# Optimization experiments

Hardware: AMD Instinct MI355X
Metric: run time of the kernel (lower is better)

The kernel has to match this reference:

```python
import jax, jax.numpy as jnp
import numpy as np

jax.config.update("jax_enable_x64", True)  # faithful int64 fixed-point requantize

B, K, N = 2048, 4096, 8192
INT32_MAX_MINUS = 2147418112  # threshold from multiply_by_quantize_mul


def setup_inputs() -> dict:
    key = jax.random.key(0)
    k1, k2, k3 = jax.random.split(key, 3)
    x = jax.random.randint(k1, (B, K), -128, 128, dtype=jnp.int8)
    weights = jax.random.randint(k2, (N, K), -128, 128, dtype=jnp.int8)
    bias = jax.random.randint(k3, (N, 1), -1024, 1024, dtype=jnp.int32)
    return {
        "x": x,
        "weights": weights,
        "bias": bias,
        "q_mantissa": 1431655765,   # ~2/3 in Q31 fixed point
        "exponent": -3,
        "output_zero_point": -5,
    }


def multiply_by_quantize_mul(x, q_mantissa, exponent):
    # Python precedence in original: (q_mantissa + (1<<15)) >> 16
    reduced_mantissa = ((q_mantissa + (1 << 15)) >> 16) if q_mantissa < INT32_MAX_MINUS else 32767
    total_shifts = 15 - exponent
    x = x * np.int64(reduced_mantissa)
    x = x + np.int64(1 << (total_shifts - 1))  # rounding term
    return jnp.right_shift(x, total_shifts)    # arithmetic shift on signed int64


def reference(x, weights, bias, q_mantissa, exponent, output_zero_point):
    # int8 GEMM accumulated in int32: result[b, n] = sum_k x[b, k] * w[n, k]
    acc = jnp.einsum("bk,nk->bn", x.astype(jnp.int32), weights.astype(jnp.int32))
    acc = acc + bias.T  # bias [N,1] -> [1,N], broadcast over batch
    acc = multiply_by_quantize_mul(acc.astype(jnp.int64), q_mantissa, exponent)
    acc = acc + np.int64(output_zero_point)
    out = jnp.clip(acc, -128, 127).astype(jnp.int8)
    return out
```

## Files before the change

### kernel.cpp

```cpp
#include <hip/hip_runtime.h>

#define DEVI __device__ __forceinline__

typedef int i32x4 __attribute__((ext_vector_type(4)));

static constexpr int Bdim = 2048;
static constexpr int Kdim = 4096;
static constexpr int Ndim = 8192;
static constexpr int BK   = 128;
static constexpr int NT   = Kdim / BK;

typedef __attribute__((address_space(1))) const unsigned int gas_t;
typedef __attribute__((address_space(3))) unsigned int las_t;

DEVI void gload_lds16(const void* g, void* l) {
    __builtin_amdgcn_global_load_lds((gas_t*)g, (las_t*)l, 16, 0, 0);
}

DEVI int pack4(i32x4 v) {
    return (v[0] & 255) | ((v[1] & 255) << 8) | ((v[2] & 255) << 16) | (v[3] << 24);
}

__global__ void pack_i32_to_i8(const int* __restrict__ in, char* __restrict__ out, int n16) {
    int i = blockIdx.x * blockDim.x + threadIdx.x;
    if (i >= n16) return;
    const i32x4* src = (const i32x4*)in + (size_t)i * 4;
    i32x4 r;
    r[0] = pack4(src[0]);
    r[1] = pack4(src[1]);
    r[2] = pack4(src[2]);
    r[3] = pack4(src[3]);
    ((i32x4*)out)[i] = r;
}

#define CFENCE asm volatile("" ::: "memory")
DEVI void bar() { CFENCE; __builtin_amdgcn_s_barrier(); CFENCE; }
#define WAITVM(N) asm volatile("s_waitcnt vmcnt(" #N ")" ::: "memory")
#define PRIO1 __builtin_amdgcn_s_setprio(1)
#define PRIO0 __builtin_amdgcn_s_setprio(0)

#define QUAD(MB)                                                                 \
    do {                                                                         \
        _Pragma("unroll") for (int mm = 0; mm < 4; ++mm)                         \
        _Pragma("unroll") for (int n = 0; n < 4; ++n)                            \
            acc[(MB) + mm][n] = __builtin_amdgcn_mfma_i32_16x16x64_i8(           \
                a[mm], b[n], acc[(MB) + mm][n], 0, 0, 0);                        \
    } while (0)

#define TILE(CUR, S1, S2, S3, S4, VM)                                                 \
    {                                                                                 \
        { _Pragma("unroll") for (int mm = 0; mm < 4; ++mm) a[mm] = rdA(CUR, 0, mm);   \
          _Pragma("unroll") for (int n = 0; n < 4; ++n)    b[n]  = rdB(CUR, 0, n);    \
          S1; bar(); PRIO1; QUAD(0); PRIO0; bar(); }                                  \
        { _Pragma("unroll") for (int mm = 0; mm < 4; ++mm) a[mm] = rdA(CUR, 0, 4+mm); \
          S2; bar(); PRIO1; QUAD(4); PRIO0; bar(); }                                  \
        { _Pragma("unroll") for (int mm = 0; mm < 4; ++mm) a[mm] = rdA(CUR, 1, mm);   \
          _Pragma("unroll") for (int n = 0; n < 4; ++n)    b[n]  = rdB(CUR, 1, n);    \
          S3; bar(); PRIO1; QUAD(0); PRIO0; bar(); }                                  \
        { _Pragma("unroll") for (int mm = 0; mm < 4; ++mm) a[mm] = rdA(CUR, 1, 4+mm); \
          S4; bar(); PRIO1; QUAD(4); PRIO0; VM; bar(); }                              \
    }

__global__ __launch_bounds__(512, 2)
void gemm8(const char* __restrict__ A8, const char* __restrict__ B8,
           const int* __restrict__ bias,
           const int* __restrict__ qm_p, const int* __restrict__ ex_p,
           const int* __restrict__ zp_p, int* __restrict__ out) {
    __shared__ i32x4 smem4[8192];
    char* smem = (char*)smem4;

    const int tid  = threadIdx.x;
    const int wid  = tid >> 6;
    const int lane = tid & 63;
    const int l15  = lane & 15;
    const int lks  = lane >> 4;
    const int wr   = wid >> 2;
    const int wc   = wid & 3;

    const int bid = blockIdx.x;
    const int swz = (bid & 7) * 32 + (bid >> 3);
    const int bm  = swz >> 5;
    const int bn  = swz & 31;
    const int arow0 = bm * 256;
    const int brow0 = bn * 256;

    const int swsel = lks ^ ((l15 >> 1) & 3);
    const int a_rd16 = (wr * 128 + l15) * 4 + swsel;
    const int b_rd16 = 4096 + (wc * 64 + l15) * 4 + swsel;

    const int st_c = (tid & 3) ^ ((tid >> 3) & 3);
    const char* agp = A8 + (size_t)(arow0 + (tid >> 2)) * Kdim + st_c * 16;
    const char* bgp = B8 + (size_t)(brow0 + (tid >> 2)) * Kdim + st_c * 16;

    auto stage = [&](int isb, int t, int ks) {
        const char* gp = (isb ? bgp : agp) + (size_t)t * BK + ks * 64;
        const int lb = (isb ? 65536 : 0) + (t & 1) * 32768 + ks * 16384 + tid * 16;
        gload_lds16(gp, &smem[lb]);
        gload_lds16(gp + (size_t)128 * Kdim, &smem[lb + 8192]);
    };
    auto rdA = [&](int buf, int ks, int m) {
        return smem4[buf * 2048 + ks * 1024 + a_rd16 + m * 64];
    };
    auto rdB = [&](int buf, int ks, int n) {
        return smem4[buf * 2048 + ks * 1024 + b_rd16 + n * 64];
    };

    i32x4 acc[8][4] = {};
    i32x4 a[4], b[4];

    stage(1, 0, 0); stage(0, 0, 0); stage(1, 0, 1); stage(0, 0, 1);
    stage(1, 1, 0); stage(0, 1, 0); stage(1, 1, 1);
    WAITVM(6);
    bar();

    int cur = 0;
    for (int t = 0; t < NT - 2; ++t) {
        TILE(cur,
             stage(0, t + 1, 1),
             stage(1, t + 2, 0),
             stage(0, t + 2, 0),
             stage(1, t + 2, 1),
             WAITVM(6));
        cur ^= 1;
    }
    TILE(cur,
         stage(0, NT - 1, 1),
         ((void)0), ((void)0), ((void)0),
         WAITVM(0));
    cur ^= 1;
    TILE(cur, ((void)0), ((void)0), ((void)0), ((void)0), ((void)0));

    const int qm = *qm_p;
    const int ex = *ex_p;
    const int zp = *zp_p;
    const int rm = (qm < 2147418112) ? ((qm + (1 << 15)) >> 16) : 32767;
    const int shifts = 15 - ex;
    const long long rnd = (shifts > 0) ? (1LL << (shifts - 1)) : 0;

    int bv[4];
#pragma unroll
    for (int n = 0; n < 4; ++n) bv[n] = bias[brow0 + wc * 64 + n * 16 + l15];

#pragma unroll
    for (int m = 0; m < 8; ++m) {
        const int row0 = arow0 + wr * 128 + m * 16 + lks * 4;
#pragma unroll
        for (int n = 0; n < 4; ++n) {
            const int col = brow0 + wc * 64 + n * 16 + l15;
#pragma unroll
            for (int j = 0; j < 4; ++j) {
                long long t = (long long)(acc[m][n][j] + bv[n]) * rm + rnd;
                t >>= shifts;
                t += zp;
                t = t < -128 ? -128 : (t > 127 ? 127 : t);
                out[(size_t)(row0 + j) * Ndim + col] = (int)t;
            }
        }
    }
}

extern "C" void kernel_launch(void* const* d_in, const int* in_sizes, int n_in,
                              void* d_out, int out_size, void* d_ws, size_t ws_size,
                              hipStream_t stream) {
    const int* x32  = (const int*)d_in[0];
    const int* w32  = (const int*)d_in[1];
    const int* bias = (const int*)d_in[2];
    const int* qm   = (const int*)d_in[3];
    const int* ex   = (const int*)d_in[4];
    const int* zp   = (const int*)d_in[5];
    int* out = (int*)d_out;

    char* xa = (char*)d_ws;
    char* wa = xa + (size_t)Bdim * Kdim;
    const int nx16 = Bdim * Kdim / 16;
    const int nw16 = Ndim * Kdim / 16;
    pack_i32_to_i8<<<(nx16 + 255) / 256, 256, 0, stream>>>(x32, xa, nx16);
    pack_i32_to_i8<<<(nw16 + 255) / 256, 256, 0, stream>>>(w32, wa, nw16);

    const int grid = (Bdim / 256) * (Ndim / 256);
    gemm8<<<grid, 512, 0, stream>>>(xa, wa, bias, qm, ex, zp, out);
}
```

Before: 105.5 us.

## Use 4-wave blocks with 128x128 per-wave tiles and simple double buffering

Replaces the 8-wave, 256x256 block kernel with a 4-wave version in which each wave computes a 128x128 output tile (8x8 MFMA accumulators), halving BK to 64. The ping-pong schedule with setprio and four sub-phases per tile becomes a plain double-buffered loop: prefetch the next tile, wait, barrier, compute, barrier. The larger per-wave tile raises register reuse of LDS fragments and removes most barriers. It costs occupancy (one block per CU, 256 accumulator VGPRs per lane) and gives up the fine-grained load/compute interleaving, so there is a risk of register spills or exposed memory latency.

```diff
diff --git a/kernel.cpp b/kernel.cpp
--- a/kernel.cpp
+++ b/kernel.cpp
@@ -7,7 +7,7 @@
 static constexpr int Bdim = 2048;
 static constexpr int Kdim = 4096;
 static constexpr int Ndim = 8192;
-static constexpr int BK   = 128;
+static constexpr int BK   = 64;
 static constexpr int NT   = Kdim / BK;
 
 typedef __attribute__((address_space(1))) const unsigned int gas_t;
@@ -36,37 +36,13 @@
 #define CFENCE asm volatile("" ::: "memory")
 DEVI void bar() { CFENCE; __builtin_amdgcn_s_barrier(); CFENCE; }
 #define WAITVM(N) asm volatile("s_waitcnt vmcnt(" #N ")" ::: "memory")
-#define PRIO1 __builtin_amdgcn_s_setprio(1)
-#define PRIO0 __builtin_amdgcn_s_setprio(0)
 
-#define QUAD(MB)                                                                 \
-    do {                                                                         \
-        _Pragma("unroll") for (int mm = 0; mm < 4; ++mm)                         \
-        _Pragma("unroll") for (int n = 0; n < 4; ++n)                            \
-            acc[(MB) + mm][n] = __builtin_amdgcn_mfma_i32_16x16x64_i8(           \
-                a[mm], b[n], acc[(MB) + mm][n], 0, 0, 0);                        \
-    } while (0)
-
-#define TILE(CUR, S1, S2, S3, S4, VM)                                                 \
-    {                                                                                 \
-        { _Pragma("unroll") for (int mm = 0; mm < 4; ++mm) a[mm] = rdA(CUR, 0, mm);   \
-          _Pragma("unroll") for (int n = 0; n < 4; ++n)    b[n]  = rdB(CUR, 0, n);    \
-          S1; bar(); PRIO1; QUAD(0); PRIO0; bar(); }                                  \
-        { _Pragma("unroll") for (int mm = 0; mm < 4; ++mm) a[mm] = rdA(CUR, 0, 4+mm); \
-          S2; bar(); PRIO1; QUAD(4); PRIO0; bar(); }                                  \
-        { _Pragma("unroll") for (int mm = 0; mm < 4; ++mm) a[mm] = rdA(CUR, 1, mm);   \
-          _Pragma("unroll") for (int n = 0; n < 4; ++n)    b[n]  = rdB(CUR, 1, n);    \
-          S3; bar(); PRIO1; QUAD(0); PRIO0; bar(); }                                  \
-        { _Pragma("unroll") for (int mm = 0; mm < 4; ++mm) a[mm] = rdA(CUR, 1, 4+mm); \
-          S4; bar(); PRIO1; QUAD(4); PRIO0; VM; bar(); }                              \
-    }
-
-__global__ __launch_bounds__(512, 2)
-void gemm8(const char* __restrict__ A8, const char* __restrict__ B8,
-           const int* __restrict__ bias,
-           const int* __restrict__ qm_p, const int* __restrict__ ex_p,
-           const int* __restrict__ zp_p, int* __restrict__ out) {
-    __shared__ i32x4 smem4[8192];
+__global__ __launch_bounds__(256, 1)
+void gemm11(const char* __restrict__ A8, const char* __restrict__ B8,
+            const int* __restrict__ bias,
+            const int* __restrict__ qm_p, const int* __restrict__ ex_p,
+            const int* __restrict__ zp_p, int* __restrict__ out) {
+    __shared__ i32x4 smem4[4096];
     char* smem = (char*)smem4;
 
     const int tid  = threadIdx.x;
@@ -74,8 +50,8 @@
     const int lane = tid & 63;
     const int l15  = lane & 15;
     const int lks  = lane >> 4;
-    const int wr   = wid >> 2;
-    const int wc   = wid & 3;
+    const int wr   = wid >> 1;
+    const int wc   = wid & 1;
 
     const int bid = blockIdx.x;
     const int swz = (bid & 7) * 32 + (bid >> 3);
@@ -85,50 +61,51 @@
     const int brow0 = bn * 256;
 
     const int swsel = lks ^ ((l15 >> 1) & 3);
-    const int a_rd16 = (wr * 128 + l15) * 4 + swsel;
-    const int b_rd16 = 4096 + (wc * 64 + l15) * 4 + swsel;
 
     const int st_c = (tid & 3) ^ ((tid >> 3) & 3);
     const char* agp = A8 + (size_t)(arow0 + (tid >> 2)) * Kdim + st_c * 16;
     const char* bgp = B8 + (size_t)(brow0 + (tid >> 2)) * Kdim + st_c * 16;
 
-    auto stage = [&](int isb, int t, int ks) {
-        const char* gp = (isb ? bgp : agp) + (size_t)t * BK + ks * 64;
-        const int lb = (isb ? 65536 : 0) + (t & 1) * 32768 + ks * 16384 + tid * 16;
-        gload_lds16(gp, &smem[lb]);
-        gload_lds16(gp + (size_t)128 * Kdim, &smem[lb + 8192]);
-    };
-    auto rdA = [&](int buf, int ks, int m) {
-        return smem4[buf * 2048 + ks * 1024 + a_rd16 + m * 64];
-    };
-    auto rdB = [&](int buf, int ks, int n) {
-        return smem4[buf * 2048 + ks * 1024 + b_rd16 + n * 64];
+    auto stage = [&](int t) {
+        const size_t ko = (size_t)t * BK;
+        const int lb = (t & 1) * 32768 + tid * 16;
+#pragma unroll
+        for (int j = 0; j < 4; ++j) {
+            gload_lds16(agp + ko + (size_t)(j * 64) * Kdim, &smem[lb + j * 4096]);
+            gload_lds16(bgp + ko + (size_t)(j * 64) * Kdim, &smem[lb + 16384 + j * 4096]);
+        }
     };
 
-    i32x4 acc[8][4] = {};
-    i32x4 a[4], b[4];
+    i32x4 acc[8][8] = {};
 
-    stage(1, 0, 0); stage(0, 0, 0); stage(1, 0, 1); stage(0, 0, 1);
-    stage(1, 1, 0); stage(0, 1, 0); stage(1, 1, 1);
-    WAITVM(6);
+    auto compute = [&](int t) {
+        const int buf = (t & 1) * 2048;
+        i32x4 a[8], b[8];
+#pragma unroll
+        for (int n = 0; n < 8; ++n)
+            b[n] = smem4[buf + 1024 + (wc * 128 + n * 16 + l15) * 4 + swsel];
+#pragma unroll
+        for (int m = 0; m < 8; ++m)
+            a[m] = smem4[buf + (wr * 128 + m * 16 + l15) * 4 + swsel];
+#pragma unroll
+        for (int m = 0; m < 8; ++m)
+#pragma unroll
+            for (int n = 0; n < 8; ++n)
+                acc[m][n] = __builtin_amdgcn_mfma_i32_16x16x64_i8(
+                    a[m], b[n], acc[m][n], 0, 0, 0);
+    };
+
+    stage(0);
+    for (int t = 0; t < NT - 1; ++t) {
+        stage(t + 1);
+        WAITVM(8);
+        bar();
+        compute(t);
+        bar();
+    }
+    WAITVM(0);
     bar();
-
-    int cur = 0;
-    for (int t = 0; t < NT - 2; ++t) {
-        TILE(cur,
-             stage(0, t + 1, 1),
-             stage(1, t + 2, 0),
-             stage(0, t + 2, 0),
-             stage(1, t + 2, 1),
-             WAITVM(6));
-        cur ^= 1;
-    }
-    TILE(cur,
-         stage(0, NT - 1, 1),
-         ((void)0), ((void)0), ((void)0),
-         WAITVM(0));
-    cur ^= 1;
-    TILE(cur, ((void)0), ((void)0), ((void)0), ((void)0), ((void)0));
+    compute(NT - 1);
 
     const int qm = *qm_p;
     const int ex = *ex_p;
@@ -137,16 +114,16 @@
     const int shifts = 15 - ex;
     const long long rnd = (shifts > 0) ? (1LL << (shifts - 1)) : 0;
 
-    int bv[4];
+    int bv[8];
 #pragma unroll
-    for (int n = 0; n < 4; ++n) bv[n] = bias[brow0 + wc * 64 + n * 16 + l15];
+    for (int n = 0; n < 8; ++n) bv[n] = bias[brow0 + wc * 128 + n * 16 + l15];
 
 #pragma unroll
     for (int m = 0; m < 8; ++m) {
         const int row0 = arow0 + wr * 128 + m * 16 + lks * 4;
 #pragma unroll
-        for (int n = 0; n < 4; ++n) {
-            const int col = brow0 + wc * 64 + n * 16 + l15;
+        for (int n = 0; n < 8; ++n) {
+            const int col = brow0 + wc * 128 + n * 16 + l15;
 #pragma unroll
             for (int j = 0; j < 4; ++j) {
                 long long t = (long long)(acc[m][n][j] + bv[n]) * rm + rnd;
@@ -178,5 +155,5 @@
     pack_i32_to_i8<<<(nw16 + 255) / 256, 256, 0, stream>>>(w32, wa, nw16);
 
     const int grid = (Bdim / 256) * (Ndim / 256);
-    gemm8<<<grid, 512, 0, stream>>>(xa, wa, bias, qm, ex, zp, out);
+    gemm11<<<grid, 256, 0, stream>>>(xa, wa, bias, qm, ex, zp, out);
 }
```

Measured after the change: 121.0 us. +14.7%, slower.

## Restructure K-loop with register double-buffered LDS reads and whole-tile staging

Applied to the files above, without the earlier changes.

Replaces the four-phase tile schedule, which put barriers around every MFMA quad and interleaved small global->LDS stages, with a loop that issues a whole K-tile of global->LDS loads at once and only two barriers per tile. LDS fragment reads are double-buffered in registers (a0/a1, b0/b1), so the next fragment loads while the current quad of MFMAs runs. The s_setprio priority hints are dropped. The aim is to cut barrier overhead and hide LDS latency behind MFMAs. In exchange it uses more VGPRs, and global loads are now bunched into one burst per tile instead of spread across the tile.

```diff
diff --git a/kernel.cpp b/kernel.cpp
--- a/kernel.cpp
+++ b/kernel.cpp
@@ -36,36 +36,25 @@
 #define CFENCE asm volatile("" ::: "memory")
 DEVI void bar() { CFENCE; __builtin_amdgcn_s_barrier(); CFENCE; }
 #define WAITVM(N) asm volatile("s_waitcnt vmcnt(" #N ")" ::: "memory")
-#define PRIO1 __builtin_amdgcn_s_setprio(1)
-#define PRIO0 __builtin_amdgcn_s_setprio(0)
 
-#define QUAD(MB)                                                                 \
+#define QUAD(MB, A, B)                                                           \
     do {                                                                         \
         _Pragma("unroll") for (int mm = 0; mm < 4; ++mm)                         \
         _Pragma("unroll") for (int n = 0; n < 4; ++n)                            \
             acc[(MB) + mm][n] = __builtin_amdgcn_mfma_i32_16x16x64_i8(           \
-                a[mm], b[n], acc[(MB) + mm][n], 0, 0, 0);                        \
+                (A)[mm], (B)[n], acc[(MB) + mm][n], 0, 0, 0);                    \
     } while (0)
 
-#define TILE(CUR, S1, S2, S3, S4, VM)                                                 \
-    {                                                                                 \
-        { _Pragma("unroll") for (int mm = 0; mm < 4; ++mm) a[mm] = rdA(CUR, 0, mm);   \
-          _Pragma("unroll") for (int n = 0; n < 4; ++n)    b[n]  = rdB(CUR, 0, n);    \
-          S1; bar(); PRIO1; QUAD(0); PRIO0; bar(); }                                  \
-        { _Pragma("unroll") for (int mm = 0; mm < 4; ++mm) a[mm] = rdA(CUR, 0, 4+mm); \
-          S2; bar(); PRIO1; QUAD(4); PRIO0; bar(); }                                  \
-        { _Pragma("unroll") for (int mm = 0; mm < 4; ++mm) a[mm] = rdA(CUR, 1, mm);   \
-          _Pragma("unroll") for (int n = 0; n < 4; ++n)    b[n]  = rdB(CUR, 1, n);    \
-          S3; bar(); PRIO1; QUAD(0); PRIO0; bar(); }                                  \
-        { _Pragma("unroll") for (int mm = 0; mm < 4; ++mm) a[mm] = rdA(CUR, 1, 4+mm); \
-          S4; bar(); PRIO1; QUAD(4); PRIO0; VM; bar(); }                              \
-    }
+#define LD_A(DST, BUF, KS, H)                                                    \
+    _Pragma("unroll") for (int mm = 0; mm < 4; ++mm) (DST)[mm] = rdA(BUF, KS, (H) + mm)
+#define LD_B(DST, BUF, KS)                                                       \
+    _Pragma("unroll") for (int n = 0; n < 4; ++n) (DST)[n] = rdB(BUF, KS, n)
 
 __global__ __launch_bounds__(512, 2)
-void gemm8(const char* __restrict__ A8, const char* __restrict__ B8,
-           const int* __restrict__ bias,
-           const int* __restrict__ qm_p, const int* __restrict__ ex_p,
-           const int* __restrict__ zp_p, int* __restrict__ out) {
+void gemm12(const char* __restrict__ A8, const char* __restrict__ B8,
+            const int* __restrict__ bias,
+            const int* __restrict__ qm_p, const int* __restrict__ ex_p,
+            const int* __restrict__ zp_p, int* __restrict__ out) {
     __shared__ i32x4 smem4[8192];
     char* smem = (char*)smem4;
 
@@ -92,11 +81,19 @@
     const char* agp = A8 + (size_t)(arow0 + (tid >> 2)) * Kdim + st_c * 16;
     const char* bgp = B8 + (size_t)(brow0 + (tid >> 2)) * Kdim + st_c * 16;
 
-    auto stage = [&](int isb, int t, int ks) {
-        const char* gp = (isb ? bgp : agp) + (size_t)t * BK + ks * 64;
-        const int lb = (isb ? 65536 : 0) + (t & 1) * 32768 + ks * 16384 + tid * 16;
-        gload_lds16(gp, &smem[lb]);
-        gload_lds16(gp + (size_t)128 * Kdim, &smem[lb + 8192]);
+    auto stageTile = [&](int t) {
+        const int base = (t & 1) * 32768;
+        const size_t ko = (size_t)t * BK;
+#pragma unroll
+        for (int ks = 0; ks < 2; ++ks) {
+            const char* ga = agp + ko + ks * 64;
+            const char* gb = bgp + ko + ks * 64;
+            const int lb = base + ks * 16384 + tid * 16;
+            gload_lds16(ga,                       &smem[lb]);
+            gload_lds16(ga + (size_t)128 * Kdim,  &smem[lb + 8192]);
+            gload_lds16(gb,                       &smem[65536 + lb]);
+            gload_lds16(gb + (size_t)128 * Kdim,  &smem[65536 + lb + 8192]);
+        }
     };
     auto rdA = [&](int buf, int ks, int m) {
         return smem4[buf * 2048 + ks * 1024 + a_rd16 + m * 64];
@@ -106,29 +103,39 @@
     };
 
     i32x4 acc[8][4] = {};
-    i32x4 a[4], b[4];
+    i32x4 a0[4], a1[4], b0[4], b1[4];
 
-    stage(1, 0, 0); stage(0, 0, 0); stage(1, 0, 1); stage(0, 0, 1);
-    stage(1, 1, 0); stage(0, 1, 0); stage(1, 1, 1);
-    WAITVM(6);
+    stageTile(0);
+    stageTile(1);
+    WAITVM(8);
     bar();
+    LD_A(a0, 0, 0, 0);
+    LD_B(b0, 0, 0);
 
-    int cur = 0;
-    for (int t = 0; t < NT - 2; ++t) {
-        TILE(cur,
-             stage(0, t + 1, 1),
-             stage(1, t + 2, 0),
-             stage(0, t + 2, 0),
-             stage(1, t + 2, 1),
-             WAITVM(6));
-        cur ^= 1;
+    for (int t = 0; t < NT; ++t) {
+        const int buf = t & 1;
+        LD_A(a1, buf, 0, 4);
+        QUAD(0, a0, b0);
+        LD_A(a0, buf, 1, 0);
+        LD_B(b1, buf, 1);
+        QUAD(4, a1, b0);
+        LD_A(a1, buf, 1, 4);
+        QUAD(0, a0, b1);
+        QUAD(4, a1, b1);
+
+        bar();
+        if (t + 2 < NT) {
+            stageTile(t + 2);
+            WAITVM(8);
+        } else {
+            WAITVM(0);
+        }
+        bar();
+        if (t + 1 < NT) {
+            LD_A(a0, buf ^ 1, 0, 0);
+            LD_B(b0, buf ^ 1, 0);
+        }
     }
-    TILE(cur,
-         stage(0, NT - 1, 1),
-         ((void)0), ((void)0), ((void)0),
-         WAITVM(0));
-    cur ^= 1;
-    TILE(cur, ((void)0), ((void)0), ((void)0), ((void)0), ((void)0));
 
     const int qm = *qm_p;
     const int ex = *ex_p;
@@ -178,5 +185,5 @@
     pack_i32_to_i8<<<(nw16 + 255) / 256, 256, 0, stream>>>(w32, wa, nw16);
 
     const int grid = (Bdim / 256) * (Ndim / 256);
-    gemm8<<<grid, 512, 0, stream>>>(xa, wa, bias, qm, ex, zp, out);
+    gemm12<<<grid, 512, 0, stream>>>(xa, wa, bias, qm, ex, zp, out);
 }
```

Measured after the change: 107.7 us. 1.02x slower.

## Restructure GEMM main loop into two k-phases with one barrier each

Applied to the files above, without the earlier changes.

The k-loop goes from four sub-phases per tile, each bracketed by two barriers, to two phases per tile. Each phase loads all 8 A fragments and 4 B fragments, issues 32 MFMAs and ends with a single barrier. Global-to-LDS staging is regrouped so that A and B of the same k-slice are issued together, with the wait counts adjusted to match. The goal is to cut barrier overhead and give the scheduler longer MFMA runs. In exchange it keeps more fragment registers live, which waves_per_eu(2,2) is meant to contain, and leaves less slack in the staging and wait ordering.

```diff
diff --git a/kernel.cpp b/kernel.cpp
--- a/kernel.cpp
+++ b/kernel.cpp
@@ -39,33 +39,30 @@
 #define PRIO1 __builtin_amdgcn_s_setprio(1)
 #define PRIO0 __builtin_amdgcn_s_setprio(0)
 
-#define QUAD(MB)                                                                 \
+#define QUAD(MB, A, B)                                                           \
     do {                                                                         \
         _Pragma("unroll") for (int mm = 0; mm < 4; ++mm)                         \
         _Pragma("unroll") for (int n = 0; n < 4; ++n)                            \
             acc[(MB) + mm][n] = __builtin_amdgcn_mfma_i32_16x16x64_i8(           \
-                a[mm], b[n], acc[(MB) + mm][n], 0, 0, 0);                        \
+                (A)[mm], (B)[n], acc[(MB) + mm][n], 0, 0, 0);                    \
     } while (0)
 
-#define TILE(CUR, S1, S2, S3, S4, VM)                                                 \
-    {                                                                                 \
-        { _Pragma("unroll") for (int mm = 0; mm < 4; ++mm) a[mm] = rdA(CUR, 0, mm);   \
-          _Pragma("unroll") for (int n = 0; n < 4; ++n)    b[n]  = rdB(CUR, 0, n);    \
-          S1; bar(); PRIO1; QUAD(0); PRIO0; bar(); }                                  \
-        { _Pragma("unroll") for (int mm = 0; mm < 4; ++mm) a[mm] = rdA(CUR, 0, 4+mm); \
-          S2; bar(); PRIO1; QUAD(4); PRIO0; bar(); }                                  \
-        { _Pragma("unroll") for (int mm = 0; mm < 4; ++mm) a[mm] = rdA(CUR, 1, mm);   \
-          _Pragma("unroll") for (int n = 0; n < 4; ++n)    b[n]  = rdB(CUR, 1, n);    \
-          S3; bar(); PRIO1; QUAD(0); PRIO0; bar(); }                                  \
-        { _Pragma("unroll") for (int mm = 0; mm < 4; ++mm) a[mm] = rdA(CUR, 1, 4+mm); \
-          S4; bar(); PRIO1; QUAD(4); PRIO0; VM; bar(); }                              \
+#define PHASE(CUR, KS, STG, VM)                                                  \
+    {                                                                            \
+        _Pragma("unroll") for (int mm = 0; mm < 8; ++mm) a[mm] = rdA(CUR, KS, mm); \
+        _Pragma("unroll") for (int n = 0; n < 4; ++n)    b[n]  = rdB(CUR, KS, n);  \
+        STG;                                                                     \
+        PRIO1; QUAD(0, a, b); QUAD(4, a + 4, b); PRIO0;                          \
+        VM;                                                                      \
+        bar();                                                                   \
     }
 
+__attribute__((amdgpu_waves_per_eu(2, 2)))
 __global__ __launch_bounds__(512, 2)
-void gemm8(const char* __restrict__ A8, const char* __restrict__ B8,
-           const int* __restrict__ bias,
-           const int* __restrict__ qm_p, const int* __restrict__ ex_p,
-           const int* __restrict__ zp_p, int* __restrict__ out) {
+void gemm13(const char* __restrict__ A8, const char* __restrict__ B8,
+            const int* __restrict__ bias,
+            const int* __restrict__ qm_p, const int* __restrict__ ex_p,
+            const int* __restrict__ zp_p, int* __restrict__ out) {
     __shared__ i32x4 smem4[8192];
     char* smem = (char*)smem4;
 
@@ -106,29 +103,31 @@
     };
 
     i32x4 acc[8][4] = {};
-    i32x4 a[4], b[4];
+    i32x4 a[8], b[4];
 
-    stage(1, 0, 0); stage(0, 0, 0); stage(1, 0, 1); stage(0, 0, 1);
-    stage(1, 1, 0); stage(0, 1, 0); stage(1, 1, 1);
-    WAITVM(6);
+    stage(0, 0, 0); stage(1, 0, 0);
+    stage(0, 0, 1); stage(1, 0, 1);
+    stage(0, 1, 0); stage(1, 1, 0);
+    WAITVM(4);
     bar();
 
-    int cur = 0;
-    for (int t = 0; t < NT - 2; ++t) {
-        TILE(cur,
-             stage(0, t + 1, 1),
-             stage(1, t + 2, 0),
-             stage(0, t + 2, 0),
-             stage(1, t + 2, 1),
-             WAITVM(6));
-        cur ^= 1;
+    int t = 0;
+    for (; t < NT - 2; ++t) {
+        const int buf = t & 1;
+        PHASE(buf, 0, (stage(0, t + 1, 1), stage(1, t + 1, 1)), ((void)0));
+        PHASE(buf, 1, (stage(0, t + 2, 0), stage(1, t + 2, 0)), WAITVM(4));
     }
-    TILE(cur,
-         stage(0, NT - 1, 1),
-         ((void)0), ((void)0), ((void)0),
-         WAITVM(0));
-    cur ^= 1;
-    TILE(cur, ((void)0), ((void)0), ((void)0), ((void)0), ((void)0));
+    {
+        const int buf = t & 1;
+        PHASE(buf, 0, (stage(0, t + 1, 1), stage(1, t + 1, 1)), ((void)0));
+        PHASE(buf, 1, ((void)0), WAITVM(0));
+    }
+    ++t;
+    {
+        const int buf = t & 1;
+        PHASE(buf, 0, ((void)0), ((void)0));
+        PHASE(buf, 1, ((void)0), ((void)0));
+    }
 
     const int qm = *qm_p;
     const int ex = *ex_p;
@@ -149,11 +148,11 @@
             const int col = brow0 + wc * 64 + n * 16 + l15;
 #pragma unroll
             for (int j = 0; j < 4; ++j) {
-                long long t = (long long)(acc[m][n][j] + bv[n]) * rm + rnd;
-                t >>= shifts;
-                t += zp;
-                t = t < -128 ? -128 : (t > 127 ? 127 : t);
-                out[(size_t)(row0 + j) * Ndim + col] = (int)t;
+                long long v = (long long)(acc[m][n][j] + bv[n]) * rm + rnd;
+                v >>= shifts;
+                v += zp;
+                v = v < -128 ? -128 : (v > 127 ? 127 : v);
+                out[(size_t)(row0 + j) * Ndim + col] = (int)v;
             }
         }
     }
@@ -178,5 +177,5 @@
     pack_i32_to_i8<<<(nw16 + 255) / 256, 256, 0, stream>>>(w32, wa, nw16);
 
     const int grid = (Bdim / 256) * (Ndim / 256);
-    gemm8<<<grid, 512, 0, stream>>>(xa, wa, bias, qm, ex, zp, out);
+    gemm13<<<grid, 512, 0, stream>>>(xa, wa, bias, qm, ex, zp, out);
 }
```

Measured after the change: 102.9 us. -2.4%, faster.
